# Performance work log

Measured on AMD Instinct MI355X. Metric: run time of the kernel, lower is better.

Reference implementation:

```python
import math
import jax, jax.numpy as jnp
import numpy as np

B, C, NX, NY = 8, 16, 512, 512
N = 16384
N_RES, NH, S = 90, 5, 0.5


def _normal(x, mu, s):
    # exp(-0.5*((x-mu)/s)^2) / (sqrt(s^2) * sqrt(2*pi))  -- matches torch helper
    return jnp.exp(-0.5 * ((x - mu) / s) ** 2) / (jnp.sqrt(s * s) * math.sqrt(2.0 * math.pi))


def setup_inputs() -> dict:
    key = jax.random.key(0)
    k1, k2 = jax.random.split(key)
    x = jax.random.normal(k1, (B, C, NX, NY), dtype=jnp.float32)
    coords = jax.random.uniform(k2, (B, N, 2), dtype=jnp.float32)
    nh_m = (NH - 1) / 2 + 0.5
    pixel_offset_normal = jnp.linspace(nh_m, -nh_m, N_RES, dtype=jnp.float32)
    pixel_offset_indices = jnp.linspace(-(NH - 1) // 2, (NH - 1) // 2, NH, dtype=jnp.float32)
    s = jnp.float32(S)
    return {"x": x, "coords": coords, "s": s,
            "pixel_offset_normal": pixel_offset_normal,
            "pixel_offset_indices": pixel_offset_indices}


def reference(x, coords, s, pixel_offset_normal, pixel_offset_indices):
    b, n, _ = coords.shape
    _, c, nx, ny = x.shape
    nh = pixel_offset_indices.shape[0]

    # continuous positions in pixel space
    px = coords[:, :, 1] * (nx - 1)   # [b,n]
    py = coords[:, :, 0] * (ny - 1)
    rpx, rpy = jnp.round(px), jnp.round(py)

    # gaussian weights integrated over sub-pixel resolution (n_res samples -> nh bins)
    # NOTE: torch code clamps both axes with x.shape[-2] (=nx); replicated faithfully.
    pxo = jnp.clip(rpx[..., None] - pixel_offset_normal, 0.0, nx)   # [b,n,n_res]
    pyo = jnp.clip(rpy[..., None] - pixel_offset_normal, 0.0, nx)
    wx = _normal(pxo, px[..., None], s).reshape(b, n, nh, -1).sum(-1)  # [b,n,nh]
    wy = _normal(pyo, py[..., None], s).reshape(b, n, nh, -1).sum(-1)
    w2d = wx[..., :, None] * wy[..., None, :]                          # [b,n,nh,nh]
    w2d = w2d / w2d.reshape(b, n, -1).sum(-1)[..., None, None]

    # integer neighborhood indices (both axes clamped with nx-1, as in torch code)
    ix = jnp.clip(jnp.round(rpx[..., None] - pixel_offset_indices), 0, nx - 1).astype(jnp.int32)  # [b,n,nh]
    iy = jnp.clip(jnp.round(rpy[..., None] - pixel_offset_indices), 0, nx - 1).astype(jnp.int32)

    # per-batch gather of nh x nh neighborhoods (equivalent to torch's BxB gather + diagonal)
    flat = (ix[..., :, None] * ny + iy[..., None, :]).reshape(b, n * nh * nh)  # [b, n*nh*nh]
    xf = x.reshape(b, c, nx * ny)
    g = jax.vmap(lambda xi, idx: xi[:, idx])(xf, flat)       # [b,c,n*nh*nh]
    g = g.reshape(b, c, n, nh, nh)

    out = (g * w2d[:, None]).reshape(b, c, n, nh * nh).sum(-1)  # [b,c,n]
    return out
```

## Files before the change

kernel.cpp:

```cpp
#include <hip/hip_runtime.h>

#define BV    8
#define CV    16
#define NXV   512
#define NYV   512
#define NV    16384
#define NRES  90
#define NHV   5
#define TPB   256

#define NPTS  (BV * NV)
#define TSH   6
#define TDIM  (NXV >> TSH)
#define NBUCKB (TDIM * TDIM)
#define NBUCK  (BV * NBUCKB)

#define CPG   2
#define NCG   (CV / CPG)
#define RROWS 68
#define RCOLS 72
#define RSEG  (RCOLS / 4)
#define SEGP  19
#define SLOTS_PER_CH (RROWS * SEGP)
#define SLOTS (CPG * SLOTS_PER_CH)
#define CHB   (SLOTS_PER_CH * 16)
#define ROWB  (SEGP * 16)

#if __has_builtin(__builtin_amdgcn_exp2f)
#define EXP2 __builtin_amdgcn_exp2f
#else
#define EXP2 exp2f
#endif

__global__ void zero_counts_kernel(int* __restrict__ counts) {
    counts[threadIdx.x] = 0;
}

__device__ __forceinline__ int bucket_key(float rpx, float rpy, int i) {
    const int tr = ((int)rpx) >> TSH;
    const int tc = ((int)rpy) >> TSH;
    return (i >> 14) * NBUCKB + tr * TDIM + tc;
}

__global__ __launch_bounds__(TPB) void bucket_count_kernel(
    const float* __restrict__ coords, int* __restrict__ counts)
{
    const int i = blockIdx.x * TPB + threadIdx.x;
    const float2 cd = *(const float2*)(coords + (size_t)i * 2);
    const float rpx = rintf(cd.y * (float)(NXV - 1));
    const float rpy = rintf(cd.x * (float)(NYV - 1));
    atomicAdd(&counts[bucket_key(rpx, rpy, i)], 1);
}

__global__ __launch_bounds__(NBUCK) void scan_kernel(
    const int* __restrict__ counts, int* __restrict__ starts,
    int* __restrict__ cursors)
{
    __shared__ int sm[NBUCK];
    const int tid = threadIdx.x;
    const int v = counts[tid];
    sm[tid] = v;
    __syncthreads();
    #pragma unroll
    for (int off = 1; off < NBUCK; off <<= 1) {
        int t = sm[tid];
        if (tid >= off) t += sm[tid - off];
        __syncthreads();
        sm[tid] = t;
        __syncthreads();
    }
    const int e = sm[tid] - v;
    starts[tid]  = e;
    cursors[tid] = e;
}

__global__ __launch_bounds__(TPB) void scatter_weights_kernel(
    const float* __restrict__ coords,
    const float* __restrict__ s_ptr,
    const float* __restrict__ offn,
    const float* __restrict__ offi,
    int* __restrict__ cursors,
    float4* __restrict__ w8a, float4* __restrict__ w8b,
    float4* __restrict__ wx4, int4* __restrict__ off4,
    float4* __restrict__ misc, int* __restrict__ posOf)
{
    const int i = blockIdx.x * TPB + threadIdx.x;

    const float2 cd = *(const float2*)(coords + (size_t)i * 2);
    const float px  = cd.y * (float)(NXV - 1);
    const float py  = cd.x * (float)(NYV - 1);
    const float rpx = rintf(px);
    const float rpy = rintf(py);

    const int pos = atomicAdd(&cursors[bucket_key(rpx, rpy, i)], 1);
    posOf[i] = pos;

    const float s = s_ptr[0];
    const float k = -0.72134752044448169f / (s * s);

    float wx[NHV], wy[NHV];
    float sx = 0.f, sy = 0.f;
    #pragma unroll
    for (int h = 0; h < NHV; ++h) {
        float ax = 0.f, ay = 0.f;
        #pragma unroll 6
        for (int t = 0; t < NRES / NHV; ++t) {
            const float off = offn[h * (NRES / NHV) + t];
            const float vx = fminf(fmaxf(rpx - off, 0.f), (float)NXV);
            const float vy = fminf(fmaxf(rpy - off, 0.f), (float)NXV);
            const float dx = vx - px;
            const float dy = vy - py;
            ax += EXP2(k * dx * dx);
            ay += EXP2(k * dy * dy);
        }
        wx[h] = ax; wy[h] = ay;
        sx += ax;  sy += ay;
    }
    const float inv = 1.0f / (sx * sy);

    int ix[NHV], iy[NHV];
    #pragma unroll
    for (int h = 0; h < NHV; ++h) {
        const float fo = offi[h];
        ix[h] = (int)fminf(fmaxf(rintf(rpx - fo), 0.f), (float)(NXV - 1));
        iy[h] = (int)fminf(fmaxf(rintf(rpy - fo), 0.f), (float)(NXV - 1));
    }

    const int a = min(iy[NHV - 1] & ~3, NYV - 8);

    float w8[8];
    #pragma unroll
    for (int kk = 0; kk < 8; ++kk) {
        float w = 0.f;
        #pragma unroll
        for (int j = 0; j < NHV; ++j)
            w += (iy[j] - a == kk) ? wy[j] * inv : 0.f;
        w8[kk] = w;
    }

    w8a[pos] = make_float4(w8[0], w8[1], w8[2], w8[3]);
    w8b[pos] = make_float4(w8[4], w8[5], w8[6], w8[7]);
    wx4[pos] = make_float4(wx[0], wx[1], wx[2], wx[3]);
    off4[pos] = make_int4((ix[0] * NYV + a) * 4, (ix[1] * NYV + a) * 4,
                          (ix[2] * NYV + a) * 4, (ix[3] * NYV + a) * 4);
    misc[pos] = make_float4(wx[4], __int_as_float((ix[4] * NYV + a) * 4),
                            0.f, 0.f);
}

__global__ __launch_bounds__(TPB) void tile_gather_kernel(
    const float* __restrict__ x,
    const int* __restrict__ starts, const int* __restrict__ ends,
    const float4* __restrict__ w8a, const float4* __restrict__ w8b,
    const float4* __restrict__ wx4, const int4* __restrict__ off4,
    const float4* __restrict__ misc,
    float* __restrict__ tmp)
{
    __shared__ float4 lds[SLOTS];

    const int bid = blockIdx.x;
    const int cg  = blockIdx.y;
    const int b   = bid >> 6;
    const int tr  = (bid >> 3) & (TDIM - 1);
    const int tc  = bid & (TDIM - 1);
    const int r0  = tr << TSH, c0 = tc << TSH;
    const int R0  = min(max(r0 - 2, 0), NXV - RROWS);
    const int W0  = min(max(c0 - 4, 0), NYV - RCOLS);

    const int tid = threadIdx.x;
    const char* bx = (const char*)x + ((size_t)(b * CV + cg * CPG) << 20);

    for (int sslot = tid; sslot < SLOTS; sslot += TPB) {
        const int ch  = sslot / SLOTS_PER_CH;
        const int rem = sslot - ch * SLOTS_PER_CH;
        const int row = rem / SEGP;
        const int seg = rem - row * SEGP;
        if (seg < RSEG)
            lds[sslot] = *(const float4*)(bx + ((size_t)ch << 20)
                          + ((size_t)(R0 + row) << 11) + (W0 << 2) + (seg << 4));
    }
    __syncthreads();

    const int s0    = starts[bid];
    const int total = (ends[bid] - s0) << 1;
    const char* ldsb = (const char*)lds;
    float* tout = tmp + (size_t)cg * (NPTS * CPG);

    for (int item = tid; item < total; item += TPB) {
        const int p   = s0 + (item >> 1);
        const int chl = item & (CPG - 1);

        const float4 wa = w8a[p];
        const float4 wb = w8b[p];
        const float4 wr = wx4[p];
        const int4   o4 = off4[p];
        const float4 ms = misc[p];
        const float  we = ms.x;
        const int    oe = __float_as_int(ms.y);

        const int basech = chl * CHB - R0 * ROWB - (W0 << 2);

        float acc = 0.f;
#define ROW(OFF, WROW) {                                                     \
        const int lo = basech + ((OFF) >> 11) * ROWB + ((OFF) & 2047);       \
        const float4 va = *(const float4*)(ldsb + lo);                       \
        const float4 vb = *(const float4*)(ldsb + lo + 16);                  \
        const float rs = va.x * wa.x + va.y * wa.y + va.z * wa.z +           \
                         va.w * wa.w + vb.x * wb.x + vb.y * wb.y +           \
                         vb.z * wb.z + vb.w * wb.w;                          \
        acc = fmaf(WROW, rs, acc); }

        ROW(o4.x, wr.x)
        ROW(o4.y, wr.y)
        ROW(o4.z, wr.z)
        ROW(o4.w, wr.w)
        ROW(oe,   we)
#undef ROW

        tout[(size_t)p * CPG + chl] = acc;
    }
}

__global__ __launch_bounds__(TPB) void transpose_kernel(
    const float* __restrict__ tmp, const int* __restrict__ posOf,
    float* __restrict__ out)
{
    const int idx = blockIdx.x * TPB + threadIdx.x;
    const int n = idx & (NV - 1);
    const int c = (idx >> 14) & (CV - 1);
    const int b = idx >> 18;
    const int p = posOf[(b << 14) | n];
    out[idx] = tmp[(size_t)(c >> 1) * (NPTS * CPG) + (size_t)p * CPG + (c & 1)];
}

extern "C" void kernel_launch(void* const* d_in, const int* in_sizes, int n_in,
                              void* d_out, int out_size, void* d_ws, size_t ws_size,
                              hipStream_t stream) {
    const float* x      = (const float*)d_in[0];
    const float* coords = (const float*)d_in[1];
    const float* s_ptr  = (const float*)d_in[2];
    const float* offn   = (const float*)d_in[3];
    const float* offi   = (const float*)d_in[4];
    float* out = (float*)d_out;

    char* w = (char*)d_ws;
    float4* w8a  = (float4*)w;  w += (size_t)NPTS * 16;
    float4* w8b  = (float4*)w;  w += (size_t)NPTS * 16;
    float4* wx4  = (float4*)w;  w += (size_t)NPTS * 16;
    int4*   off4 = (int4*)w;    w += (size_t)NPTS * 16;
    float4* misc = (float4*)w;  w += (size_t)NPTS * 16;
    float*  tmp  = (float*)w;   w += (size_t)NPTS * CV * 4;
    int*    posOf = (int*)w;    w += (size_t)NPTS * 4;
    int*    counts  = (int*)w;  w += (size_t)NBUCK * 4;
    int*    starts  = (int*)w;  w += (size_t)NBUCK * 4;
    int*    cursors = (int*)w;

    zero_counts_kernel<<<dim3(1), dim3(NBUCK), 0, stream>>>(counts);
    bucket_count_kernel<<<dim3(NPTS / TPB), dim3(TPB), 0, stream>>>(coords, counts);
    scan_kernel<<<dim3(1), dim3(NBUCK), 0, stream>>>(counts, starts, cursors);
    scatter_weights_kernel<<<dim3(NPTS / TPB), dim3(TPB), 0, stream>>>(
        coords, s_ptr, offn, offi, cursors, w8a, w8b, wx4, off4, misc, posOf);

    dim3 grid(NBUCK, NCG, 1);
    tile_gather_kernel<<<grid, dim3(TPB), 0, stream>>>(
        x, starts, cursors, w8a, w8b, wx4, off4, misc, tmp);

    transpose_kernel<<<dim3(NPTS * CV / TPB), dim3(TPB), 0, stream>>>(
        tmp, posOf, out);
}
```

Measured before the change: 312.9 us.

## Fuse transpose into tile gather with one channel per block and direct output writes

The separate transpose kernel and its tmp/posOf buffers are removed. The original point index is stored in the misc record, so the gather kernel writes each result straight to its final [b,c,n] location. Each block now handles a single channel, with a smaller unpadded LDS tile, an unrolled tile load and a launch-bounds occupancy hint. This drops one kernel launch and a full round trip through an intermediate buffer. In exchange, output writes are scattered rather than coalesced, and per-point weight records are re-read across 16 channel blocks instead of 8.

```diff
diff --git a/kernel.cpp b/kernel.cpp
--- a/kernel.cpp
+++ b/kernel.cpp
@@ -15,16 +15,10 @@
 #define NBUCKB (TDIM * TDIM)
 #define NBUCK  (BV * NBUCKB)
 
-#define CPG   2
-#define NCG   (CV / CPG)
 #define RROWS 68
-#define RCOLS 72
-#define RSEG  (RCOLS / 4)
-#define SEGP  19
-#define SLOTS_PER_CH (RROWS * SEGP)
-#define SLOTS (CPG * SLOTS_PER_CH)
-#define CHB   (SLOTS_PER_CH * 16)
-#define ROWB  (SEGP * 16)
+#define RSEG  18
+#define ROWB  (RSEG * 16)
+#define SLOTS (RROWS * RSEG)
 
 #if __has_builtin(__builtin_amdgcn_exp2f)
 #define EXP2 __builtin_amdgcn_exp2f
@@ -82,7 +76,7 @@
     int* __restrict__ cursors,
     float4* __restrict__ w8a, float4* __restrict__ w8b,
     float4* __restrict__ wx4, int4* __restrict__ off4,
-    float4* __restrict__ misc, int* __restrict__ posOf)
+    float4* __restrict__ misc)
 {
     const int i = blockIdx.x * TPB + threadIdx.x;
 
@@ -93,7 +87,6 @@
     const float rpy = rintf(py);
 
     const int pos = atomicAdd(&cursors[bucket_key(rpx, rpy, i)], 1);
-    posOf[i] = pos;
 
     const float s = s_ptr[0];
     const float k = -0.72134752044448169f / (s * s);
@@ -144,51 +137,49 @@
     off4[pos] = make_int4((ix[0] * NYV + a) * 4, (ix[1] * NYV + a) * 4,
                           (ix[2] * NYV + a) * 4, (ix[3] * NYV + a) * 4);
     misc[pos] = make_float4(wx[4], __int_as_float((ix[4] * NYV + a) * 4),
-                            0.f, 0.f);
-}
-
-__global__ __launch_bounds__(TPB) void tile_gather_kernel(
+                            __int_as_float(i), 0.f);
+}
+
+__global__ __launch_bounds__(TPB, 8) void tile_gather_kernel(
     const float* __restrict__ x,
     const int* __restrict__ starts, const int* __restrict__ ends,
     const float4* __restrict__ w8a, const float4* __restrict__ w8b,
     const float4* __restrict__ wx4, const int4* __restrict__ off4,
     const float4* __restrict__ misc,
-    float* __restrict__ tmp)
+    float* __restrict__ out)
 {
     __shared__ float4 lds[SLOTS];
 
     const int bid = blockIdx.x;
-    const int cg  = blockIdx.y;
+    const int c   = blockIdx.y;
     const int b   = bid >> 6;
     const int tr  = (bid >> 3) & (TDIM - 1);
     const int tc  = bid & (TDIM - 1);
     const int r0  = tr << TSH, c0 = tc << TSH;
     const int R0  = min(max(r0 - 2, 0), NXV - RROWS);
-    const int W0  = min(max(c0 - 4, 0), NYV - RCOLS);
+    const int W0  = min(max(c0 - 4, 0), NYV - RSEG * 4);
 
     const int tid = threadIdx.x;
-    const char* bx = (const char*)x + ((size_t)(b * CV + cg * CPG) << 20);
-
-    for (int sslot = tid; sslot < SLOTS; sslot += TPB) {
-        const int ch  = sslot / SLOTS_PER_CH;
-        const int rem = sslot - ch * SLOTS_PER_CH;
-        const int row = rem / SEGP;
-        const int seg = rem - row * SEGP;
-        if (seg < RSEG)
-            lds[sslot] = *(const float4*)(bx + ((size_t)ch << 20)
-                          + ((size_t)(R0 + row) << 11) + (W0 << 2) + (seg << 4));
+    const char* bx = (const char*)x + ((size_t)(b * CV + c) << 20);
+
+    #pragma unroll
+    for (int kk = 0; kk < (SLOTS + TPB - 1) / TPB; ++kk) {
+        const int slot = tid + kk * TPB;
+        if (slot < SLOTS) {
+            const int row = slot / RSEG;
+            const int seg = slot - row * RSEG;
+            lds[slot] = *(const float4*)(bx + ((size_t)(R0 + row) << 11)
+                                            + (W0 << 2) + (seg << 4));
+        }
     }
     __syncthreads();
 
-    const int s0    = starts[bid];
-    const int total = (ends[bid] - s0) << 1;
+    const int s0 = starts[bid];
+    const int e1 = ends[bid];
     const char* ldsb = (const char*)lds;
-    float* tout = tmp + (size_t)cg * (NPTS * CPG);
-
-    for (int item = tid; item < total; item += TPB) {
-        const int p   = s0 + (item >> 1);
-        const int chl = item & (CPG - 1);
-
+    const int base0 = -R0 * ROWB - (W0 << 2);
+
+    for (int p = s0 + tid; p < e1; p += TPB) {
         const float4 wa = w8a[p];
         const float4 wb = w8b[p];
         const float4 wr = wx4[p];
@@ -196,12 +187,12 @@
         const float4 ms = misc[p];
         const float  we = ms.x;
         const int    oe = __float_as_int(ms.y);
-
-        const int basech = chl * CHB - R0 * ROWB - (W0 << 2);
+        const int    i  = __float_as_int(ms.z);
+        const int    n  = i & (NV - 1);
 
         float acc = 0.f;
 #define ROW(OFF, WROW) {                                                     \
-        const int lo = basech + ((OFF) >> 11) * ROWB + ((OFF) & 2047);       \
+        const int lo = base0 + ((OFF) >> 11) * ROWB + ((OFF) & 2047);        \
         const float4 va = *(const float4*)(ldsb + lo);                       \
         const float4 vb = *(const float4*)(ldsb + lo + 16);                  \
         const float rs = va.x * wa.x + va.y * wa.y + va.z * wa.z +           \
@@ -216,20 +207,8 @@
         ROW(oe,   we)
 #undef ROW
 
-        tout[(size_t)p * CPG + chl] = acc;
-    }
-}
-
-__global__ __launch_bounds__(TPB) void transpose_kernel(
-    const float* __restrict__ tmp, const int* __restrict__ posOf,
-    float* __restrict__ out)
-{
-    const int idx = blockIdx.x * TPB + threadIdx.x;
-    const int n = idx & (NV - 1);
-    const int c = (idx >> 14) & (CV - 1);
-    const int b = idx >> 18;
-    const int p = posOf[(b << 14) | n];
-    out[idx] = tmp[(size_t)(c >> 1) * (NPTS * CPG) + (size_t)p * CPG + (c & 1)];
+        out[(((size_t)(b * CV + c)) << 14) + n] = acc;
+    }
 }
 
 extern "C" void kernel_launch(void* const* d_in, const int* in_sizes, int n_in,
@@ -248,8 +227,6 @@
     float4* wx4  = (float4*)w;  w += (size_t)NPTS * 16;
     int4*   off4 = (int4*)w;    w += (size_t)NPTS * 16;
     float4* misc = (float4*)w;  w += (size_t)NPTS * 16;
-    float*  tmp  = (float*)w;   w += (size_t)NPTS * CV * 4;
-    int*    posOf = (int*)w;    w += (size_t)NPTS * 4;
     int*    counts  = (int*)w;  w += (size_t)NBUCK * 4;
     int*    starts  = (int*)w;  w += (size_t)NBUCK * 4;
     int*    cursors = (int*)w;
@@ -258,12 +235,9 @@
     bucket_count_kernel<<<dim3(NPTS / TPB), dim3(TPB), 0, stream>>>(coords, counts);
     scan_kernel<<<dim3(1), dim3(NBUCK), 0, stream>>>(counts, starts, cursors);
     scatter_weights_kernel<<<dim3(NPTS / TPB), dim3(TPB), 0, stream>>>(
-        coords, s_ptr, offn, offi, cursors, w8a, w8b, wx4, off4, misc, posOf);
-
-    dim3 grid(NBUCK, NCG, 1);
+        coords, s_ptr, offn, offi, cursors, w8a, w8b, wx4, off4, misc);
+
+    dim3 grid(NBUCK, CV, 1);
     tile_gather_kernel<<<grid, dim3(TPB), 0, stream>>>(
-        x, starts, cursors, w8a, w8b, wx4, off4, misc, tmp);
-
-    transpose_kernel<<<dim3(NPTS * CV / TPB), dim3(TPB), 0, stream>>>(
-        tmp, posOf, out);
-}
+        x, starts, cursors, w8a, w8b, wx4, off4, misc, out);
+}
```

Measured after the change: 300.9 us. -3.8%, faster.
